# Kernel tuning notes

Hardware: AMD Instinct MI355X
Metric: run time of the kernel (lower is better)

The kernel has to match this reference:

```python
import jax, jax.numpy as jnp
import numpy as np

N = 50000      # nodes
E = 800000     # edges (before self loops)
IN = 61        # input node features
H = 256        # hidden
HEADS = 8
C = H // HEADS # per-head channels = 32
L = 4          # GAT layers
EPS = 1e-5


def setup_inputs() -> dict:
    key = jax.random.key(0)
    ks = jax.random.split(key, 10)
    s = 0.05
    return {
        "x": jax.random.normal(ks[0], (N, IN), jnp.float32),
        "edge_index": jax.random.randint(ks[1], (2, E), 0, N),
        "in_W": jax.random.normal(ks[2], (IN, H), jnp.float32) * s,
        "in_b": jnp.zeros((H,), jnp.float32),
        "in_gamma": jnp.ones((H,), jnp.float32),
        "in_beta": jnp.zeros((H,), jnp.float32),
        "Ws": jax.random.normal(ks[3], (L, H, H), jnp.float32) * s,
        "att_src": jax.random.normal(ks[4], (L, HEADS, C), jnp.float32) * s,
        "att_dst": jax.random.normal(ks[5], (L, HEADS, C), jnp.float32) * s,
        "conv_b": jnp.zeros((L, H), jnp.float32),
        "bn_gamma": jnp.ones((L, H), jnp.float32),
        "bn_beta": jnp.zeros((L, H), jnp.float32),
        "mean_W": jax.random.normal(ks[6], (H, 1), jnp.float32) * s,
        "mean_b": jnp.zeros((1,), jnp.float32),
        "lv_W": jax.random.normal(ks[7], (H, 1), jnp.float32) * s,
        "lv_b": jnp.zeros((1,), jnp.float32),
    }


def _bn(h, gamma, beta):
    # training-mode BatchNorm1d: batch stats, biased variance
    mu = h.mean(axis=0)
    var = jnp.var(h, axis=0)
    return (h - mu) * jax.lax.rsqrt(var + EPS) * gamma + beta


def _gat_layer(h, src, dst, W, a_src, a_dst, bias):
    # h: [N,H] -> z: [N,HEADS,C]
    z = (h @ W).reshape(N, HEADS, C)
    e_src = jnp.einsum('nhc,hc->nh', z, a_src)  # [N,HEADS]
    e_dst = jnp.einsum('nhc,hc->nh', z, a_dst)
    e = jax.nn.leaky_relu(e_src[src] + e_dst[dst], 0.2)  # [Etot,HEADS]
    # segment softmax over destination neighborhoods
    emax = jax.ops.segment_max(e, dst, num_segments=N)
    p = jnp.exp(e - emax[dst])
    denom = jax.ops.segment_sum(p, dst, num_segments=N)
    alpha = p / denom[dst]
    # weighted scatter-aggregate of per-edge messages
    out = jax.ops.segment_sum(z[src] * alpha[:, :, None], dst, num_segments=N)
    return out.reshape(N, H) + bias


def reference(x, edge_index, in_W, in_b, in_gamma, in_beta, Ws, att_src,
              att_dst, conv_b, bn_gamma, bn_beta, mean_W, mean_b, lv_W, lv_b):
    loops = jnp.arange(N, dtype=edge_index.dtype)
    src = jnp.concatenate([edge_index[0], loops])  # add_self_loops=True
    dst = jnp.concatenate([edge_index[1], loops])
    # input projection: Linear -> BN -> ReLU (dropout off, deterministic)
    h = jax.nn.relu(_bn(x @ in_W + in_b, in_gamma, in_beta))
    for i in range(L):
        res = h
        h = _gat_layer(h, src, dst, Ws[i], att_src[i], att_dst[i], conv_b[i])
        h = jax.nn.relu(_bn(h, bn_gamma[i], bn_beta[i])) + res
    mean = (h @ mean_W + mean_b)[:, 0]
    log_var = jnp.clip((h @ lv_W + lv_b)[:, 0], -10.0, 10.0)
    return (mean, log_var)
```

## Files before the change

kernel.cpp:

```cpp
#include <hip/hip_runtime.h>

#define NN 50000
#define EE 800000
#define ETOT 850000
#define KIN 61
#define HH 256
#define NH 8
#define CC 32
#define LL 4
#define SCAN_NBLK 49

typedef __attribute__((ext_vector_type(8))) short bf16x8;
typedef __attribute__((ext_vector_type(4))) float f32x4;

__device__ __forceinline__ unsigned short f2b(float f) {
    unsigned u = __builtin_bit_cast(unsigned, f);
    u += 0x7fffu + ((u >> 16) & 1u);
    return (unsigned short)(u >> 16);
}
__device__ __forceinline__ float b2f(unsigned short h) {
    unsigned u = ((unsigned)h) << 16;
    return __builtin_bit_cast(float, u);
}

__device__ __forceinline__ void gload16(const void* g, void* l) {
    __builtin_amdgcn_global_load_lds(
        (const __attribute__((address_space(1))) void*)g,
        (__attribute__((address_space(3))) void*)l, 16, 0, 0);
}


__global__ __launch_bounds__(256) void edge_hist(const int* __restrict__ ei,
                                                 int* __restrict__ counts) {
    int e = blockIdx.x * 256 + threadIdx.x;
    if (e >= ETOT) return;
    int d = (e < EE) ? ei[EE + e] : (e - EE);
    atomicAdd(&counts[d], 1);
}

__global__ __launch_bounds__(256) void scan1(const int* __restrict__ counts,
                                             int* __restrict__ tmp,
                                             int* __restrict__ bsums) {
    __shared__ int lds[256];
    int b = blockIdx.x, t = threadIdx.x;
    int base = b * 1024 + t * 4;
    int v0 = 0, v1 = 0, v2 = 0, v3 = 0;
    if (base + 0 < NN) v0 = counts[base + 0];
    if (base + 1 < NN) v1 = counts[base + 1];
    if (base + 2 < NN) v2 = counts[base + 2];
    if (base + 3 < NN) v3 = counts[base + 3];
    int s = v0 + v1 + v2 + v3;
    lds[t] = s;
    __syncthreads();
    for (int off = 1; off < 256; off <<= 1) {
        int x = (t >= off) ? lds[t - off] : 0;
        __syncthreads();
        lds[t] += x;
        __syncthreads();
    }
    int run = lds[t] - s;
    if (t == 255) bsums[b] = lds[255];
    run += v0; if (base + 0 < NN) tmp[base + 0] = run;
    run += v1; if (base + 1 < NN) tmp[base + 1] = run;
    run += v2; if (base + 2 < NN) tmp[base + 2] = run;
    run += v3; if (base + 3 < NN) tmp[base + 3] = run;
}

__global__ void scan2(int* __restrict__ bsums) {
    if (threadIdx.x == 0) {
        int acc = 0;
        for (int i = 0; i < SCAN_NBLK; ++i) { int t = bsums[i]; bsums[i] = acc; acc += t; }
    }
}

__global__ __launch_bounds__(256) void scan3(const int* __restrict__ tmp,
                                             const int* __restrict__ bsums,
                                             const int* __restrict__ counts,
                                             int* __restrict__ rowptr,
                                             int* __restrict__ cursor) {
    int i = blockIdx.x * 256 + threadIdx.x;
    if (i >= NN) return;
    int incl = tmp[i] + bsums[i >> 10];
    rowptr[i + 1] = incl;
    cursor[i] = incl - counts[i];
    if (i == 0) rowptr[0] = 0;
}

__global__ __launch_bounds__(256) void edge_scatter(const int* __restrict__ ei,
                                                    int* __restrict__ cursor,
                                                    int* __restrict__ ssrc) {
    int e = blockIdx.x * 256 + threadIdx.x;
    if (e >= ETOT) return;
    int s, d;
    if (e < EE) { s = ei[e]; d = ei[EE + e]; } else { s = d = e - EE; }
    int pos = atomicAdd(&cursor[d], 1);
    ssrc[pos] = s;
}

__global__ __launch_bounds__(256) void sort_rows(const int* __restrict__ rowptr,
                                                 int* __restrict__ ssrc) {
    int wid = (blockIdx.x * 256 + threadIdx.x) >> 6;
    int lane = threadIdx.x & 63;
    if (wid >= NN) return;
    int beg = rowptr[wid], end = rowptr[wid + 1];
    int L = end - beg;
    if (L > 64) return;
    int v = (lane < L) ? ssrc[beg + lane] : 0x7fffffff;
#pragma unroll
    for (int k = 2; k <= 64; k <<= 1) {
#pragma unroll
        for (int j = k >> 1; j > 0; j >>= 1) {
            int partner = __shfl_xor(v, j);
            bool up = ((lane & k) == 0);
            bool keepMin = (up == ((lane & j) == 0));
            int mn = min(v, partner), mx = max(v, partner);
            v = keepMin ? mn : mx;
        }
    }
    if (lane < L) ssrc[beg + lane] = v;
}


__global__ __launch_bounds__(256) void prep_wt(const float* __restrict__ Ws,
                                               unsigned short* __restrict__ WT) {
    int t = blockIdx.x * 256 + threadIdx.x;
    if (t >= LL * HH * HH) return;
    int l = t >> 16, rem = t & 65535;
    int n = rem >> 8, k = rem & 255;
    WT[t] = f2b(Ws[l * 65536 + k * HH + n]);
}

__global__ __launch_bounds__(256) void prep_inwt(const float* __restrict__ in_W,
                                                 unsigned short* __restrict__ WT) {
    int t = blockIdx.x * 256 + threadIdx.x;
    if (t >= HH * 64) return;
    int n = t >> 6, k = t & 63;
    WT[t] = (k < KIN) ? f2b(in_W[k * HH + n]) : 0;
}

__global__ __launch_bounds__(256) void prep_x(const float* __restrict__ x,
                                              unsigned short* __restrict__ xb) {
    int t = blockIdx.x * 256 + threadIdx.x;
    if (t >= NN * 64) return;
    int n = t >> 6, c = t & 63;
    xb[t] = (c < KIN) ? f2b(x[n * KIN + c]) : 0;
}

template<int ZHM>
__global__ __launch_bounds__(256) void gemm_mfma(const unsigned short* __restrict__ A,
                                                 const unsigned short* __restrict__ Bt,
                                                 unsigned short* __restrict__ C,
                                                 const float* __restrict__ asl,
                                                 const float* __restrict__ adl,
                                                 float* __restrict__ esrcT,
                                                 float* __restrict__ edstT,
                                                 int M, int K) {
    __shared__ unsigned short As[128 * 64];
    __shared__ unsigned short Bs[128 * 64];
    int row0 = blockIdx.x * 128;
    int n0 = blockIdx.y * 128;
    int tid = threadIdx.x;
    int w = tid >> 6, l = tid & 63;
    int wm = w >> 1, wn = w & 1;
    int r15 = l & 15, q = l >> 4;

    f32x4 acc[4][4] = {};

    int crow = l >> 3;
    int cs   = l & 7;

    for (int kt = 0; kt < K; kt += 64) {
        if (kt) __syncthreads();
#pragma unroll
        for (int c = 0; c < 4; ++c) {
            int r = w * 32 + c * 8 + crow;
            int sg = cs ^ (r & 7);
            int ga = row0 + r; if (ga >= M) ga = M - 1;
            gload16(&A[(size_t)ga * K + kt + sg * 8], &As[(w * 32 + c * 8) * 64]);
            int gb = n0 + r;
            gload16(&Bt[(size_t)gb * K + kt + sg * 8], &Bs[(w * 32 + c * 8) * 64]);
        }
        __syncthreads();
#pragma unroll
        for (int kk = 0; kk < 2; ++kk) {
            bf16x8 aF[4], bF[4];
#pragma unroll
            for (int i = 0; i < 4; ++i) {
                int ar = wm * 64 + i * 16 + r15;
                aF[i] = *(bf16x8*)&As[ar * 64 + ((kk * 4 + q) ^ (ar & 7)) * 8];
                int br = wn * 64 + i * 16 + r15;
                bF[i] = *(bf16x8*)&Bs[br * 64 + ((kk * 4 + q) ^ (br & 7)) * 8];
            }
#pragma unroll
            for (int i = 0; i < 4; ++i)
#pragma unroll
                for (int j = 0; j < 4; ++j)
                    acc[i][j] = __builtin_amdgcn_mfma_f32_16x16x32_bf16(aF[i], bF[j], acc[i][j], 0, 0, 0);
        }
    }

#pragma unroll
    for (int i = 0; i < 4; ++i)
#pragma unroll
        for (int j = 0; j < 4; ++j) {
            int nc = n0 + wn * 64 + j * 16 + r15;
#pragma unroll
            for (int r = 0; r < 4; ++r) {
                int gr = row0 + wm * 64 + i * 16 + q * 4 + r;
                if (gr < M) {
                    if (ZHM)
                        C[(size_t)(nc >> 5) * NN * CC + (size_t)gr * CC + (nc & 31)] = f2b(acc[i][j][r]);
                    else
                        C[(size_t)gr * HH + nc] = f2b(acc[i][j][r]);
                }
            }
        }

    if constexpr (ZHM) {
        int hdbase = (n0 >> 5) + wn * 2;
        float as_[4], ad_[4];
#pragma unroll
        for (int j = 0; j < 4; ++j) {
            int idx = (hdbase + (j >> 1)) * CC + (j & 1) * 16 + r15;
            as_[j] = asl[idx];
            ad_[j] = adl[idx];
        }
#pragma unroll
        for (int h = 0; h < 2; ++h) {
#pragma unroll
            for (int i = 0; i < 4; ++i) {
                float pes[4], ped[4];
#pragma unroll
                for (int r = 0; r < 4; ++r) {
                    float v0 = b2f(f2b(acc[i][2 * h][r]));
                    float v1 = b2f(f2b(acc[i][2 * h + 1][r]));
                    pes[r] = v0 * as_[2 * h] + v1 * as_[2 * h + 1];
                    ped[r] = v0 * ad_[2 * h] + v1 * ad_[2 * h + 1];
                }
#pragma unroll
                for (int off = 1; off <= 8; off <<= 1) {
#pragma unroll
                    for (int r = 0; r < 4; ++r) {
                        pes[r] += __shfl_xor(pes[r], off);
                        ped[r] += __shfl_xor(ped[r], off);
                    }
                }
                int hd = hdbase + h;
                if (r15 < 8) {
                    int r = r15 & 3;
                    int gr = row0 + wm * 64 + i * 16 + q * 4 + r;
                    if (gr < M) {
                        if (r15 < 4) esrcT[(size_t)hd * NN + gr] = pes[r];
                        else         edstT[(size_t)hd * NN + gr] = ped[r];
                    }
                }
            }
        }
    }
}

#define MAXEB 2048
__global__ __launch_bounds__(256) void aggregate(const int* __restrict__ rowptr,
                                                 const int* __restrict__ ssrc,
                                                 const float* __restrict__ esrcT,
                                                 const float* __restrict__ edstT,
                                                 const unsigned short* __restrict__ zT,
                                                 unsigned short* __restrict__ outb,
                                                 float* __restrict__ sums) {
    __shared__ int   s_lds[MAXEB];
    __shared__ float p_lds[MAXEB];
    __shared__ int   rp_lds[33];
    __shared__ float ed_lds[32];
    __shared__ float ws1[4][8][4], ws2[4][8][4];
    int bid = blockIdx.x;
    int hd = bid & 7;
    int n0 = (bid >> 3) * 32;
    int tid = threadIdx.x;
    const float* esp = esrcT + (size_t)hd * NN;
    const unsigned short* zp = zT + (size_t)hd * NN * CC;

    if (tid <= 32) {
        int idx = n0 + tid;
        rp_lds[tid] = rowptr[idx > NN ? NN : idx];
    }
    if (tid < 32) {
        int nn = n0 + tid;
        ed_lds[tid] = (nn < NN) ? edstT[(size_t)hd * NN + nn] : 0.f;
    }
    __syncthreads();
    int beg0 = rp_lds[0];
    int total = rp_lds[32] - beg0;
    bool staged = (total <= MAXEB);
    if (staged) {
        for (int j = tid; j < total; j += 256) {
            int s = ssrc[beg0 + j];
            int jj = beg0 + j;
            int lo = 0, hi = 32;
#pragma unroll
            for (int st = 0; st < 5; ++st) {
                int mid = (lo + hi) >> 1;
                bool le = (rp_lds[mid] <= jj);
                lo = le ? mid : lo;
                hi = le ? hi : mid;
            }
            float e = esp[s] + ed_lds[lo];
            e = (e > 0.f) ? e : 0.2f * e;
            s_lds[j] = s;
            p_lds[j] = __expf(e);
        }
    }
    __syncthreads();

    int lane = tid & 63;
    int wv = tid >> 6;
    int g = lane >> 3;
    int nl = wv * 8 + g;
    int n = n0 + nl;
    int col = (lane & 7) * 4;
    bool act = n < NN;
    int jbeg = rp_lds[nl] - beg0;
    int jend = rp_lds[nl + 1] - beg0;

    float den0 = 0.f, den1 = 0.f;
    float a0 = 0.f, a1 = 0.f, a2 = 0.f, a3 = 0.f;
    float b0 = 0.f, b1 = 0.f, b2 = 0.f, b3 = 0.f;
    int j = jbeg;
    if (staged) {
        for (; j + 1 < jend; j += 2) {
            int s0 = s_lds[j], s1 = s_lds[j + 1];
            float p0 = p_lds[j], p1 = p_lds[j + 1];
            ushort4 z0 = *(const ushort4*)&zp[(size_t)(s0 * CC + col)];
            ushort4 z1 = *(const ushort4*)&zp[(size_t)(s1 * CC + col)];
            den0 += p0;
            a0 += p0 * b2f(z0.x); a1 += p0 * b2f(z0.y);
            a2 += p0 * b2f(z0.z); a3 += p0 * b2f(z0.w);
            den1 += p1;
            b0 += p1 * b2f(z1.x); b1 += p1 * b2f(z1.y);
            b2 += p1 * b2f(z1.z); b3 += p1 * b2f(z1.w);
        }
        if (j < jend) {
            int s0 = s_lds[j];
            float p0 = p_lds[j];
            ushort4 z0 = *(const ushort4*)&zp[(size_t)(s0 * CC + col)];
            den0 += p0;
            a0 += p0 * b2f(z0.x); a1 += p0 * b2f(z0.y);
            a2 += p0 * b2f(z0.z); a3 += p0 * b2f(z0.w);
        }
    } else {
        float ed = act ? ed_lds[nl] : 0.f;
        for (; j + 1 < jend; j += 2) {
            int s0 = ssrc[beg0 + j], s1 = ssrc[beg0 + j + 1];
            float es0 = esp[s0], es1 = esp[s1];
            ushort4 z0 = *(const ushort4*)&zp[(size_t)(s0 * CC + col)];
            ushort4 z1 = *(const ushort4*)&zp[(size_t)(s1 * CC + col)];
            float e0 = es0 + ed; e0 = (e0 > 0.f) ? e0 : 0.2f * e0;
            float e1 = es1 + ed; e1 = (e1 > 0.f) ? e1 : 0.2f * e1;
            float p0 = __expf(e0);
            float p1 = __expf(e1);
            den0 += p0;
            a0 += p0 * b2f(z0.x); a1 += p0 * b2f(z0.y);
            a2 += p0 * b2f(z0.z); a3 += p0 * b2f(z0.w);
            den1 += p1;
            b0 += p1 * b2f(z1.x); b1 += p1 * b2f(z1.y);
            b2 += p1 * b2f(z1.z); b3 += p1 * b2f(z1.w);
        }
        if (j < jend) {
            int s0 = ssrc[beg0 + j];
            float es0 = esp[s0];
            ushort4 z0 = *(const ushort4*)&zp[(size_t)(s0 * CC + col)];
            float e0 = es0 + ed; e0 = (e0 > 0.f) ? e0 : 0.2f * e0;
            float p0 = __expf(e0);
            den0 += p0;
            a0 += p0 * b2f(z0.x); a1 += p0 * b2f(z0.y);
            a2 += p0 * b2f(z0.z); a3 += p0 * b2f(z0.w);
        }
    }
    float v0 = 0.f, v1 = 0.f, v2 = 0.f, v3 = 0.f;
    if (act) {
        float inv = 1.f / (den0 + den1);
        ushort4 o;
        o.x = f2b((a0 + b0) * inv); o.y = f2b((a1 + b1) * inv);
        o.z = f2b((a2 + b2) * inv); o.w = f2b((a3 + b3) * inv);
        *(ushort4*)&outb[(size_t)n * HH + hd * CC + col] = o;
        v0 = b2f(o.x); v1 = b2f(o.y); v2 = b2f(o.z); v3 = b2f(o.w);
    }
    float q0 = v0 * v0, q1 = v1 * v1, q2 = v2 * v2, q3 = v3 * v3;
#pragma unroll
    for (int off = 8; off <= 32; off <<= 1) {
        v0 += __shfl_xor(v0, off); v1 += __shfl_xor(v1, off);
        v2 += __shfl_xor(v2, off); v3 += __shfl_xor(v3, off);
        q0 += __shfl_xor(q0, off); q1 += __shfl_xor(q1, off);
        q2 += __shfl_xor(q2, off); q3 += __shfl_xor(q3, off);
    }
    if (g == 0) {
        int slot = lane & 7;
        ws1[wv][slot][0] = v0; ws1[wv][slot][1] = v1;
        ws1[wv][slot][2] = v2; ws1[wv][slot][3] = v3;
        ws2[wv][slot][0] = q0; ws2[wv][slot][1] = q1;
        ws2[wv][slot][2] = q2; ws2[wv][slot][3] = q3;
    }
    __syncthreads();
    if (tid < 32) {
        int slot = tid & 7, k = tid >> 3;
        float s1v = ws1[0][slot][k] + ws1[1][slot][k] + ws1[2][slot][k] + ws1[3][slot][k];
        float s2v = ws2[0][slot][k] + ws2[1][slot][k] + ws2[2][slot][k] + ws2[3][slot][k];
        int ch = hd * CC + slot * 4 + k;
        atomicAdd(&sums[ch], s1v);
        atomicAdd(&sums[HH + ch], s2v);
    }
}

__global__ __launch_bounds__(256) void col_stats(const unsigned short* __restrict__ X,
                                                 float* __restrict__ sums) {
    int c = threadIdx.x;
    int rows_per_block = (NN + gridDim.x - 1) / gridDim.x;
    int r0 = blockIdx.x * rows_per_block;
    int r1 = min(NN, r0 + rows_per_block);
    float s = 0.f, q = 0.f;
    for (int r = r0; r < r1; ++r) {
        float v = b2f(X[(size_t)r * HH + c]);
        s += v; q += v * v;
    }
    atomicAdd(&sums[c], s);
    atomicAdd(&sums[HH + c], q);
}

__global__ __launch_bounds__(256) void bn_relu_add(const unsigned short* __restrict__ X,
                                                   const float* __restrict__ sums,
                                                   const float* __restrict__ gamma,
                                                   const float* __restrict__ beta,
                                                   const unsigned short* __restrict__ res,
                                                   unsigned short* __restrict__ outb) {
    int i = blockIdx.x * 256 + threadIdx.x;
    if (i >= NN * 64) return;
    int c4 = (i & 63) * 4;
    const float invN = 1.f / NN;
    ushort4 u = *(const ushort4*)(X + (size_t)i * 4);
    float v0 = b2f(u.x), v1 = b2f(u.y), v2 = b2f(u.z), v3 = b2f(u.w);
    float4 s1 = *(const float4*)&sums[c4];
    float4 s2 = *(const float4*)&sums[HH + c4];
    float4 gm = *(const float4*)&gamma[c4];
    float4 bt = *(const float4*)&beta[c4];
    float mn0 = s1.x * invN, mn1 = s1.y * invN, mn2 = s1.z * invN, mn3 = s1.w * invN;
    float rs0 = rsqrtf(fmaxf(s2.x * invN - mn0 * mn0, 0.f) + 1e-5f);
    float rs1 = rsqrtf(fmaxf(s2.y * invN - mn1 * mn1, 0.f) + 1e-5f);
    float rs2 = rsqrtf(fmaxf(s2.z * invN - mn2 * mn2, 0.f) + 1e-5f);
    float rs3 = rsqrtf(fmaxf(s2.w * invN - mn3 * mn3, 0.f) + 1e-5f);
    float r0 = fmaxf((v0 - mn0) * rs0 * gm.x + bt.x, 0.f);
    float r1 = fmaxf((v1 - mn1) * rs1 * gm.y + bt.y, 0.f);
    float r2 = fmaxf((v2 - mn2) * rs2 * gm.z + bt.z, 0.f);
    float r3 = fmaxf((v3 - mn3) * rs3 * gm.w + bt.w, 0.f);
    if (res) {
        ushort4 rv = *(const ushort4*)(res + (size_t)i * 4);
        r0 += b2f(rv.x); r1 += b2f(rv.y); r2 += b2f(rv.z); r3 += b2f(rv.w);
    }
    ushort4 ob;
    ob.x = f2b(r0); ob.y = f2b(r1); ob.z = f2b(r2); ob.w = f2b(r3);
    *(ushort4*)(outb + (size_t)i * 4) = ob;
}

__global__ __launch_bounds__(256) void out_proj(const unsigned short* __restrict__ h,
                                                const float* __restrict__ mW,
                                                const float* __restrict__ mb,
                                                const float* __restrict__ lW,
                                                const float* __restrict__ lb,
                                                float* __restrict__ out) {
    int wid = (blockIdx.x * 256 + threadIdx.x) >> 6;
    int lane = threadIdx.x & 63;
    if (wid >= NN) return;
    ushort4 hv = *(const ushort4*)&h[(size_t)wid * HH + lane * 4];
    float h0 = b2f(hv.x), h1 = b2f(hv.y), h2 = b2f(hv.z), h3 = b2f(hv.w);
    float4 wv = *(const float4*)&mW[lane * 4];
    float4 lv = *(const float4*)&lW[lane * 4];
    float sm = h0 * wv.x + h1 * wv.y + h2 * wv.z + h3 * wv.w;
    float sl = h0 * lv.x + h1 * lv.y + h2 * lv.z + h3 * lv.w;
    for (int off = 32; off > 0; off >>= 1) {
        sm += __shfl_down(sm, off);
        sl += __shfl_down(sl, off);
    }
    if (lane == 0) {
        out[wid] = sm + mb[0];
        float l = sl + lb[0];
        out[NN + wid] = fminf(10.f, fmaxf(-10.f, l));
    }
}

extern "C" void kernel_launch(void* const* d_in, const int* in_sizes, int n_in,
                              void* d_out, int out_size, void* d_ws, size_t ws_size,
                              hipStream_t stream) {
    const float* x        = (const float*)d_in[0];
    const int*   ei       = (const int*)d_in[1];
    const float* in_W     = (const float*)d_in[2];
    const float* in_gamma = (const float*)d_in[4];
    const float* in_beta  = (const float*)d_in[5];
    const float* Ws       = (const float*)d_in[6];
    const float* att_src  = (const float*)d_in[7];
    const float* att_dst  = (const float*)d_in[8];
    const float* bn_gamma = (const float*)d_in[10];
    const float* bn_beta  = (const float*)d_in[11];
    const float* mean_W   = (const float*)d_in[12];
    const float* mean_b   = (const float*)d_in[13];
    const float* lv_W     = (const float*)d_in[14];
    const float* lv_b     = (const float*)d_in[15];
    float* out = (float*)d_out;

    char* p = (char*)d_ws;
    unsigned short* z    = (unsigned short*)p; p += (size_t)NN * HH * 2;
    unsigned short* hb   = (unsigned short*)p; p += (size_t)NN * HH * 2;
    unsigned short* aggb = (unsigned short*)p; p += (size_t)NN * HH * 2;
    float* esrcT = (float*)p;                  p += (size_t)NN * NH * 4;
    float* edstT = (float*)p;                  p += (size_t)NN * NH * 4;
    float* sums = (float*)p;                   p += 512 * 4;
    unsigned short* WT   = (unsigned short*)p; p += (size_t)LL * HH * HH * 2;
    unsigned short* inWT = (unsigned short*)p; p += (size_t)HH * 64 * 2;
    int* counts = (int*)p;                     p += (size_t)NN * 4;
    int* rowptr = (int*)p;                     p += (size_t)(NN + 1) * 4;
    int* cursor = (int*)p;                     p += (size_t)NN * 4;
    int* ssrc   = (int*)p;                     p += (size_t)ETOT * 4;
    int* bsums  = (int*)p;                     p += 64 * 4;
    unsigned short* xb = aggb;

    hipMemsetAsync(counts, 0, NN * sizeof(int), stream);
    edge_hist<<<(ETOT + 255) / 256, 256, 0, stream>>>(ei, counts);
    scan1<<<SCAN_NBLK, 256, 0, stream>>>(counts, cursor, bsums);
    scan2<<<1, 64, 0, stream>>>(bsums);
    scan3<<<(NN + 255) / 256, 256, 0, stream>>>(cursor, bsums, counts, rowptr, cursor);
    edge_scatter<<<(ETOT + 255) / 256, 256, 0, stream>>>(ei, cursor, ssrc);
    sort_rows<<<(NN * 64 + 255) / 256, 256, 0, stream>>>(rowptr, ssrc);

    prep_wt<<<(LL * HH * HH + 255) / 256, 256, 0, stream>>>(Ws, WT);
    prep_inwt<<<(HH * 64 + 255) / 256, 256, 0, stream>>>(in_W, inWT);
    prep_x<<<(NN * 64 + 255) / 256, 256, 0, stream>>>(x, xb);

    {
        dim3 g((NN + 127) / 128, 2);
        gemm_mfma<0><<<g, 256, 0, stream>>>(xb, inWT, z, nullptr, nullptr,
                                            nullptr, nullptr, NN, 64);
    }
    hipMemsetAsync(sums, 0, 512 * sizeof(float), stream);
    col_stats<<<1024, 256, 0, stream>>>(z, sums);
    bn_relu_add<<<(NN * 64 + 255) / 256, 256, 0, stream>>>(z, sums, in_gamma, in_beta,
                                                           nullptr, hb);

    for (int l = 0; l < LL; ++l) {
        const unsigned short* WTl = WT + (size_t)l * HH * HH;
        const float* asl = att_src + (size_t)l * NH * CC;
        const float* adl = att_dst + (size_t)l * NH * CC;
        const float* gl  = bn_gamma + (size_t)l * HH;
        const float* bl  = bn_beta + (size_t)l * HH;

        dim3 g((NN + 127) / 128, 2);
        gemm_mfma<1><<<g, 256, 0, stream>>>(hb, WTl, z, asl, adl, esrcT, edstT, NN, HH);
        hipMemsetAsync(sums, 0, 512 * sizeof(float), stream);
        aggregate<<<((NN + 31) / 32) * 8, 256, 0, stream>>>(rowptr, ssrc, esrcT, edstT,
                                                            z, aggb, sums);
        bn_relu_add<<<(NN * 64 + 255) / 256, 256, 0, stream>>>(aggb, sums, gl, bl, hb, hb);
    }

    out_proj<<<(NN * 64 + 255) / 256, 256, 0, stream>>>(hb, mean_W, mean_b, lv_W, lv_b, out);
}
```

Before: 717.6 us.

## Widen GEMM tile to full 256 columns and unroll aggregate gather by four

The MFMA GEMM now runs 512-thread blocks that each cover all 256 output columns for a 128-row tile. The A tile is loaded once instead of twice across two column blocks, and the grid becomes one-dimensional. In the aggregate kernel the staged gather loop is unrolled to four edges with independent accumulators for more memory-level parallelism. The unstaged path drops its two-edge unroll and becomes a single-edge loop. The larger block and doubled B tile in shared memory raise register and LDS pressure, which may lower occupancy.

```diff
diff --git a/kernel.cpp b/kernel.cpp
--- a/kernel.cpp
+++ b/kernel.cpp
@@ -147,7 +147,7 @@
 }
 
 template<int ZHM>
-__global__ __launch_bounds__(256) void gemm_mfma(const unsigned short* __restrict__ A,
+__global__ __launch_bounds__(512) void gemm_mfma(const unsigned short* __restrict__ A,
                                                  const unsigned short* __restrict__ Bt,
                                                  unsigned short* __restrict__ C,
                                                  const float* __restrict__ asl,
@@ -156,12 +156,11 @@
                                                  float* __restrict__ edstT,
                                                  int M, int K) {
     __shared__ unsigned short As[128 * 64];
-    __shared__ unsigned short Bs[128 * 64];
+    __shared__ unsigned short Bs[256 * 64];
     int row0 = blockIdx.x * 128;
-    int n0 = blockIdx.y * 128;
     int tid = threadIdx.x;
     int w = tid >> 6, l = tid & 63;
-    int wm = w >> 1, wn = w & 1;
+    int wm = w >> 2, wn = w & 3;
     int r15 = l & 15, q = l >> 4;
 
     f32x4 acc[4][4] = {};
@@ -171,14 +170,18 @@
 
     for (int kt = 0; kt < K; kt += 64) {
         if (kt) __syncthreads();
+#pragma unroll
+        for (int c = 0; c < 2; ++c) {
+            int r = w * 16 + c * 8 + crow;
+            int sg = cs ^ (r & 7);
+            int ga = row0 + r; if (ga >= M) ga = M - 1;
+            gload16(&A[(size_t)ga * K + kt + sg * 8], &As[(w * 16 + c * 8) * 64]);
+        }
 #pragma unroll
         for (int c = 0; c < 4; ++c) {
             int r = w * 32 + c * 8 + crow;
             int sg = cs ^ (r & 7);
-            int ga = row0 + r; if (ga >= M) ga = M - 1;
-            gload16(&A[(size_t)ga * K + kt + sg * 8], &As[(w * 32 + c * 8) * 64]);
-            int gb = n0 + r;
-            gload16(&Bt[(size_t)gb * K + kt + sg * 8], &Bs[(w * 32 + c * 8) * 64]);
+            gload16(&Bt[(size_t)r * K + kt + sg * 8], &Bs[(w * 32 + c * 8) * 64]);
         }
         __syncthreads();
 #pragma unroll
@@ -203,7 +206,7 @@
     for (int i = 0; i < 4; ++i)
 #pragma unroll
         for (int j = 0; j < 4; ++j) {
-            int nc = n0 + wn * 64 + j * 16 + r15;
+            int nc = wn * 64 + j * 16 + r15;
 #pragma unroll
             for (int r = 0; r < 4; ++r) {
                 int gr = row0 + wm * 64 + i * 16 + q * 4 + r;
@@ -217,7 +220,7 @@
         }
 
     if constexpr (ZHM) {
-        int hdbase = (n0 >> 5) + wn * 2;
+        int hdbase = wn * 2;
         float as_[4], ad_[4];
 #pragma unroll
         for (int j = 0; j < 4; ++j) {
@@ -321,66 +324,63 @@
     int jbeg = rp_lds[nl] - beg0;
     int jend = rp_lds[nl + 1] - beg0;
 
-    float den0 = 0.f, den1 = 0.f;
-    float a0 = 0.f, a1 = 0.f, a2 = 0.f, a3 = 0.f;
-    float b0 = 0.f, b1 = 0.f, b2 = 0.f, b3 = 0.f;
+    float d0 = 0.f, d1 = 0.f, d2 = 0.f, d3 = 0.f;
+    float a00 = 0.f, a01 = 0.f, a02 = 0.f, a03 = 0.f;
+    float a10 = 0.f, a11 = 0.f, a12 = 0.f, a13 = 0.f;
+    float a20 = 0.f, a21 = 0.f, a22 = 0.f, a23 = 0.f;
+    float a30 = 0.f, a31 = 0.f, a32 = 0.f, a33 = 0.f;
     int j = jbeg;
     if (staged) {
-        for (; j + 1 < jend; j += 2) {
-            int s0 = s_lds[j], s1 = s_lds[j + 1];
-            float p0 = p_lds[j], p1 = p_lds[j + 1];
+        for (; j + 3 < jend; j += 4) {
+            int s0 = s_lds[j], s1 = s_lds[j + 1], s2 = s_lds[j + 2], s3 = s_lds[j + 3];
+            float p0 = p_lds[j], p1 = p_lds[j + 1], p2 = p_lds[j + 2], p3 = p_lds[j + 3];
             ushort4 z0 = *(const ushort4*)&zp[(size_t)(s0 * CC + col)];
             ushort4 z1 = *(const ushort4*)&zp[(size_t)(s1 * CC + col)];
-            den0 += p0;
-            a0 += p0 * b2f(z0.x); a1 += p0 * b2f(z0.y);
-            a2 += p0 * b2f(z0.z); a3 += p0 * b2f(z0.w);
-            den1 += p1;
-            b0 += p1 * b2f(z1.x); b1 += p1 * b2f(z1.y);
-            b2 += p1 * b2f(z1.z); b3 += p1 * b2f(z1.w);
-        }
-        if (j < jend) {
+            ushort4 z2 = *(const ushort4*)&zp[(size_t)(s2 * CC + col)];
+            ushort4 z3 = *(const ushort4*)&zp[(size_t)(s3 * CC + col)];
+            d0 += p0;
+            a00 += p0 * b2f(z0.x); a01 += p0 * b2f(z0.y);
+            a02 += p0 * b2f(z0.z); a03 += p0 * b2f(z0.w);
+            d1 += p1;
+            a10 += p1 * b2f(z1.x); a11 += p1 * b2f(z1.y);
+            a12 += p1 * b2f(z1.z); a13 += p1 * b2f(z1.w);
+            d2 += p2;
+            a20 += p2 * b2f(z2.x); a21 += p2 * b2f(z2.y);
+            a22 += p2 * b2f(z2.z); a23 += p2 * b2f(z2.w);
+            d3 += p3;
+            a30 += p3 * b2f(z3.x); a31 += p3 * b2f(z3.y);
+            a32 += p3 * b2f(z3.z); a33 += p3 * b2f(z3.w);
+        }
+        for (; j < jend; ++j) {
             int s0 = s_lds[j];
             float p0 = p_lds[j];
             ushort4 z0 = *(const ushort4*)&zp[(size_t)(s0 * CC + col)];
-            den0 += p0;
-            a0 += p0 * b2f(z0.x); a1 += p0 * b2f(z0.y);
-            a2 += p0 * b2f(z0.z); a3 += p0 * b2f(z0.w);
+            d0 += p0;
+            a00 += p0 * b2f(z0.x); a01 += p0 * b2f(z0.y);
+            a02 += p0 * b2f(z0.z); a03 += p0 * b2f(z0.w);
         }
     } else {
         float ed = act ? ed_lds[nl] : 0.f;
-        for (; j + 1 < jend; j += 2) {
-            int s0 = ssrc[beg0 + j], s1 = ssrc[beg0 + j + 1];
-            float es0 = esp[s0], es1 = esp[s1];
-            ushort4 z0 = *(const ushort4*)&zp[(size_t)(s0 * CC + col)];
-            ushort4 z1 = *(const ushort4*)&zp[(size_t)(s1 * CC + col)];
-            float e0 = es0 + ed; e0 = (e0 > 0.f) ? e0 : 0.2f * e0;
-            float e1 = es1 + ed; e1 = (e1 > 0.f) ? e1 : 0.2f * e1;
-            float p0 = __expf(e0);
-            float p1 = __expf(e1);
-            den0 += p0;
-            a0 += p0 * b2f(z0.x); a1 += p0 * b2f(z0.y);
-            a2 += p0 * b2f(z0.z); a3 += p0 * b2f(z0.w);
-            den1 += p1;
-            b0 += p1 * b2f(z1.x); b1 += p1 * b2f(z1.y);
-            b2 += p1 * b2f(z1.z); b3 += p1 * b2f(z1.w);
-        }
-        if (j < jend) {
+        for (; j < jend; ++j) {
             int s0 = ssrc[beg0 + j];
             float es0 = esp[s0];
             ushort4 z0 = *(const ushort4*)&zp[(size_t)(s0 * CC + col)];
             float e0 = es0 + ed; e0 = (e0 > 0.f) ? e0 : 0.2f * e0;
             float p0 = __expf(e0);
-            den0 += p0;
-            a0 += p0 * b2f(z0.x); a1 += p0 * b2f(z0.y);
-            a2 += p0 * b2f(z0.z); a3 += p0 * b2f(z0.w);
+            d0 += p0;
+            a00 += p0 * b2f(z0.x); a01 += p0 * b2f(z0.y);
+            a02 += p0 * b2f(z0.z); a03 += p0 * b2f(z0.w);
         }
     }
     float v0 = 0.f, v1 = 0.f, v2 = 0.f, v3 = 0.f;
     if (act) {
-        float inv = 1.f / (den0 + den1);
+        float den = (d0 + d1) + (d2 + d3);
+        float inv = 1.f / den;
         ushort4 o;
-        o.x = f2b((a0 + b0) * inv); o.y = f2b((a1 + b1) * inv);
-        o.z = f2b((a2 + b2) * inv); o.w = f2b((a3 + b3) * inv);
+        o.x = f2b(((a00 + a10) + (a20 + a30)) * inv);
+        o.y = f2b(((a01 + a11) + (a21 + a31)) * inv);
+        o.z = f2b(((a02 + a12) + (a22 + a32)) * inv);
+        o.w = f2b(((a03 + a13) + (a23 + a33)) * inv);
         *(ushort4*)&outb[(size_t)n * HH + hd * CC + col] = o;
         v0 = b2f(o.x); v1 = b2f(o.y); v2 = b2f(o.z); v3 = b2f(o.w);
     }
@@ -532,11 +532,8 @@
     prep_inwt<<<(HH * 64 + 255) / 256, 256, 0, stream>>>(in_W, inWT);
     prep_x<<<(NN * 64 + 255) / 256, 256, 0, stream>>>(x, xb);
 
-    {
-        dim3 g((NN + 127) / 128, 2);
-        gemm_mfma<0><<<g, 256, 0, stream>>>(xb, inWT, z, nullptr, nullptr,
-                                            nullptr, nullptr, NN, 64);
-    }
+    gemm_mfma<0><<<(NN + 127) / 128, 512, 0, stream>>>(xb, inWT, z, nullptr, nullptr,
+                                                       nullptr, nullptr, NN, 64);
     hipMemsetAsync(sums, 0, 512 * sizeof(float), stream);
     col_stats<<<1024, 256, 0, stream>>>(z, sums);
     bn_relu_add<<<(NN * 64 + 255) / 256, 256, 0, stream>>>(z, sums, in_gamma, in_beta,
@@ -549,8 +546,8 @@
         const float* gl  = bn_gamma + (size_t)l * HH;
         const float* bl  = bn_beta + (size_t)l * HH;
 
-        dim3 g((NN + 127) / 128, 2);
-        gemm_mfma<1><<<g, 256, 0, stream>>>(hb, WTl, z, asl, adl, esrcT, edstT, NN, HH);
+        gemm_mfma<1><<<(NN + 127) / 128, 512, 0, stream>>>(hb, WTl, z, asl, adl,
+                                                           esrcT, edstT, NN, HH);
         hipMemsetAsync(sums, 0, 512 * sizeof(float), stream);
         aggregate<<<((NN + 31) / 32) * 8, 256, 0, stream>>>(rowptr, ssrc, esrcT, edstT,
                                                             z, aggb, sums);
```

Result: faster. 689.2 us (-4.0%).
